# Optimization experiments

Measured on AMD Instinct MI355X. Metric: run time of the kernel, lower is better.

Reference implementation:

```python
import jax, jax.numpy as jnp
import numpy as np

B, S, H, E = 4, 2048, 1024, 8

def setup_inputs() -> dict:
    key = jax.random.key(0)
    k1, k2, k3 = jax.random.split(key, 3)
    scale_g = 1.0 / np.sqrt(H)
    scale_e = 1.0 / np.sqrt(H)
    return {
        "x": jax.random.normal(k1, (B, S, H), dtype=jnp.float32),
        "gate_w": jax.random.normal(k2, (H, E), dtype=jnp.float32) * scale_g,
        "gate_b": jnp.zeros((E,), dtype=jnp.float32),
        "expert_w": jax.random.normal(k3, (E, H, H), dtype=jnp.float32) * scale_e,
        "expert_b": jnp.zeros((E, H), dtype=jnp.float32),
    }

def reference(x, gate_w, gate_b, expert_w, expert_b):
    b, s, h = x.shape
    tok = x.reshape(-1, h)                                  # [T, H]
    # gate: softmax over experts per token
    w = jax.nn.softmax(tok @ gate_w + gate_b, axis=-1)      # [T, E]
    # all experts applied to all tokens (dense MoE)
    eo = jnp.einsum("th,ehd->ted", tok, expert_w) + expert_b[None]  # [T, E, H]
    out = jnp.einsum("te,ted->td", w, eo)                   # [T, H]
    return out.reshape(b, s, h)
```

## Files before the change

kernel.cpp:

```cpp
#include <hip/hip_runtime.h>
#include <stdint.h>

typedef unsigned short u16;
typedef short bf8 __attribute__((ext_vector_type(8)));
typedef float f4 __attribute__((ext_vector_type(4)));
typedef _Float16 h2 __attribute__((ext_vector_type(2)));

#define TTOK 8192
#define HD   1024
#define NE   8
#define HH   (HD * HD)

static __device__ __forceinline__ u16 f2bf(float f) {
  union { float f; uint32_t u; } v; v.f = f;
  return (u16)((v.u + 0x7fffu + ((v.u >> 16) & 1u)) >> 16);
}

__global__ __launch_bounds__(256) void gate_conv_kernel(
    const float* __restrict__ x, const float* __restrict__ gw,
    const float* __restrict__ gb, float* __restrict__ wout,
    u16* __restrict__ abf)
{
  const int t    = blockIdx.x * 4 + (threadIdx.x >> 6);
  const int lane = threadIdx.x & 63;
  const float* xr = x + (size_t)t * HD;
  float p[NE];
#pragma unroll
  for (int e = 0; e < NE; ++e) p[e] = 0.f;
#pragma unroll 4
  for (int h = lane; h < HD; h += 64) {
    const float xv = xr[h];
    abf[(size_t)t * HD + h] = f2bf(xv);
    const float* g = gw + (size_t)h * NE;
#pragma unroll
    for (int e = 0; e < NE; ++e) p[e] += xv * g[e];
  }
#pragma unroll
  for (int e = 0; e < NE; ++e) {
#pragma unroll
    for (int off = 32; off > 0; off >>= 1)
      p[e] += __shfl_xor(p[e], off, 64);
    p[e] += gb[e];
  }
  float m = p[0];
#pragma unroll
  for (int e = 1; e < NE; ++e) m = fmaxf(m, p[e]);
  float s = 0.f;
#pragma unroll
  for (int e = 0; e < NE; ++e) { p[e] = expf(p[e] - m); s += p[e]; }
  const float inv = 1.f / s;
  if (lane == 0) {
#pragma unroll
    for (int e = 0; e < NE; ++e) wout[t * NE + e] = p[e] * inv;
  }
}

__global__ __launch_bounds__(256) void wconv_kernel(
    const float* __restrict__ ew, u16* __restrict__ wt)
{
  __shared__ u16 tile[64][66];
  const int e  = blockIdx.z;
  const int h0 = blockIdx.y * 64;
  const int d0 = blockIdx.x * 64;
  const int c  = threadIdx.x & 63;
  const int r0 = threadIdx.x >> 6;
  const float* src = ew + (size_t)e * HH;
  u16* dst = wt + (size_t)e * HH;
#pragma unroll
  for (int i = 0; i < 16; ++i) {
    const int r = i * 4 + r0;
    tile[r][c] = f2bf(src[(size_t)(h0 + r) * HD + d0 + c]);
  }
  __syncthreads();
#pragma unroll
  for (int i = 0; i < 16; ++i) {
    const int r = i * 4 + r0;
    dst[(size_t)(d0 + r) * HD + h0 + c] = tile[c][r];
  }
}

#define BM 256
#define BN 128
#define BK 64
#define SLOT 65536

#define MM(a_, b_, c_) __builtin_amdgcn_mfma_f32_16x16x32_bf16((a_), (b_), (c_), 0, 0, 0)

#define GL(srcp_, dstp_) __builtin_amdgcn_global_load_lds( \
    (const __attribute__((address_space(1))) void*)(srcp_), \
    (__attribute__((address_space(3))) void*)(dstp_), 16, 0, 0)

#define STAGE_A(sq_)                                                \
  {                                                                 \
    const int sk_ = ((sq_) & 15) << 6;                              \
    const u16* as_ = aSrc0 + sk_;                                   \
    char* ad_ = smem + stS + tid * 16;                              \
    GL(as_,          ad_);                                          \
    GL(as_ +  65536, ad_ +  8192);                                  \
    GL(as_ + 131072, ad_ + 16384);                                  \
    GL(as_ + 196608, ad_ + 24576);                                  \
  }
#define STAGE_B(sq_)                                                \
  {                                                                 \
    const int pn_ = (sq_) >> 4;                                     \
    const int sk_ = ((sq_) & 15) << 6;                              \
    const u16* b0_ = bSrc0 + (size_t)(2 * pn_) * HH + sk_;          \
    char* bd_ = smem + stS + 32768 + tid * 16;                      \
    GL(b0_,          bd_);                                          \
    GL(b0_ +  65536, bd_ +  8192);                                  \
    GL(b0_ + HH,          bd_ + 16384);                             \
    GL(b0_ + HH + 65536,  bd_ + 24576);                             \
  }

#define READS(aP_, bP_)                                   \
    bf8 a0  = *(const bf8*)(aP_);                         \
    bf8 a1  = *(const bf8*)((aP_) + 2048);                \
    bf8 a2  = *(const bf8*)((aP_) + 4096);                \
    bf8 a3  = *(const bf8*)((aP_) + 6144);                \
    bf8 b00 = *(const bf8*)(bP_);                         \
    bf8 b01 = *(const bf8*)((bP_) + 2048);                \
    bf8 b02 = *(const bf8*)((bP_) + 4096);                \
    bf8 b03 = *(const bf8*)((bP_) + 6144);                \
    bf8 b10 = *(const bf8*)((bP_) + 16384);               \
    bf8 b11 = *(const bf8*)((bP_) + 18432);               \
    bf8 b12 = *(const bf8*)((bP_) + 20480);               \
    bf8 b13 = *(const bf8*)((bP_) + 22528);

#define MFMA32                                            \
    acc0[0][0] = MM(a0, b00, acc0[0][0]);                 \
    acc0[1][0] = MM(a1, b00, acc0[1][0]);                 \
    acc0[2][0] = MM(a2, b00, acc0[2][0]);                 \
    acc0[3][0] = MM(a3, b00, acc0[3][0]);                 \
    acc0[0][1] = MM(a0, b01, acc0[0][1]);                 \
    acc0[1][1] = MM(a1, b01, acc0[1][1]);                 \
    acc0[2][1] = MM(a2, b01, acc0[2][1]);                 \
    acc0[3][1] = MM(a3, b01, acc0[3][1]);                 \
    acc0[0][2] = MM(a0, b02, acc0[0][2]);                 \
    acc0[1][2] = MM(a1, b02, acc0[1][2]);                 \
    acc0[2][2] = MM(a2, b02, acc0[2][2]);                 \
    acc0[3][2] = MM(a3, b02, acc0[3][2]);                 \
    acc0[0][3] = MM(a0, b03, acc0[0][3]);                 \
    acc0[1][3] = MM(a1, b03, acc0[1][3]);                 \
    acc0[2][3] = MM(a2, b03, acc0[2][3]);                 \
    acc0[3][3] = MM(a3, b03, acc0[3][3]);                 \
    acc1[0][0] = MM(a0, b10, acc1[0][0]);                 \
    acc1[1][0] = MM(a1, b10, acc1[1][0]);                 \
    acc1[2][0] = MM(a2, b10, acc1[2][0]);                 \
    acc1[3][0] = MM(a3, b10, acc1[3][0]);                 \
    acc1[0][1] = MM(a0, b11, acc1[0][1]);                 \
    acc1[1][1] = MM(a1, b11, acc1[1][1]);                 \
    acc1[2][1] = MM(a2, b11, acc1[2][1]);                 \
    acc1[3][1] = MM(a3, b11, acc1[3][1]);                 \
    acc1[0][2] = MM(a0, b12, acc1[0][2]);                 \
    acc1[1][2] = MM(a1, b12, acc1[1][2]);                 \
    acc1[2][2] = MM(a2, b12, acc1[2][2]);                 \
    acc1[3][2] = MM(a3, b12, acc1[3][2]);                 \
    acc1[0][3] = MM(a0, b13, acc1[0][3]);                 \
    acc1[1][3] = MM(a1, b13, acc1[1][3]);                 \
    acc1[2][3] = MM(a2, b13, acc1[2][3]);                 \
    acc1[3][3] = MM(a3, b13, acc1[3][3]);

#define FOLD(e0_, e1_)                                                  \
  {                                                                     \
    _Pragma("unroll")                                                   \
    for (int mi = 0; mi < 4; ++mi) {                                    \
      const int r_ = wrb + mi * 16 + lhi * 4;                           \
      float wa[4], wb[4];                                               \
      _Pragma("unroll")                                                 \
      for (int j = 0; j < 4; ++j) {                                     \
        wa[j] = wgs[(r_ + j) * 9 + (e0_)];                              \
        wb[j] = wgs[(r_ + j) * 9 + (e1_)];                              \
      }                                                                 \
      _Pragma("unroll")                                                 \
      for (int ni = 0; ni < 4; ++ni) {                                  \
        const float f0 = wa[0] * acc0[mi][ni][0] + wb[0] * acc1[mi][ni][0]; \
        const float f1 = wa[1] * acc0[mi][ni][1] + wb[1] * acc1[mi][ni][1]; \
        const float f2 = wa[2] * acc0[mi][ni][2] + wb[2] * acc1[mi][ni][2]; \
        const float f3 = wa[3] * acc0[mi][ni][3] + wb[3] * acc1[mi][ni][3]; \
        h2 t0; t0[0] = (_Float16)f0; t0[1] = (_Float16)f1;              \
        h2 t1; t1[0] = (_Float16)f2; t1[1] = (_Float16)f3;              \
        accP0[mi][ni] += t0;                                            \
        accP1[mi][ni] += t1;                                            \
        acc0[mi][ni] = fz; acc1[mi][ni] = fz;                           \
      }                                                                 \
    }                                                                   \
  }

#define BAR       __builtin_amdgcn_s_barrier();
#define LGKM0     asm volatile("s_waitcnt lgkmcnt(0)" ::: "memory");
#define VM0       asm volatile("s_waitcnt vmcnt(0)" ::: "memory");
#define PRIO1     __builtin_amdgcn_s_setprio(1);
#define PRIO0     __builtin_amdgcn_s_setprio(0);

__global__ __launch_bounds__(512, 2) void moe_gemm_kernel(
    const u16* __restrict__ A,
    const u16* __restrict__ Wt,
    const float* __restrict__ wg,
    const float* __restrict__ eb,
    float* __restrict__ out)
{
  __shared__ __attribute__((aligned(16))) char smem[2 * SLOT + 9216];
  float* wgs = (float*)(smem + 2 * SLOT);

  const int bid   = blockIdx.x;
  const int xcd   = bid & 7;
  const int local = bid >> 3;
  const int bm    = xcd * 4 + (local & 3);
  const int bn    = local >> 2;
  const int row0  = bm * BM;
  const int col0  = bn * BN;

  const int tid  = threadIdx.x;
  const int lane = tid & 63;
  const int wid  = tid >> 6;
  const int wr   = wid >> 1;
  const int wc   = wid & 1;
  const int l15  = lane & 15;
  const int lhi  = lane >> 4;
  const int wrb  = wr * 64;
  const int wcb  = wc * 64;

  const int gsl   = (lhi ^ (l15 & 7)) << 4;
  const int thrA0 = wrb * 128 + l15 * 128 + gsl;
  const int thrA1 = thrA0 ^ 64;
  const int thrB0 = 32768 + wcb * 128 + l15 * 128 + gsl;
  const int thrB1 = thrB0 ^ 64;

  const int row_in = tid >> 3;
  const int gsw    = (tid & 7) ^ (row_in & 7);
  const u16* aSrc0 = A  + (size_t)(row0 + row_in) * HD + gsw * 8;
  const u16* bSrc0 = Wt + (size_t)(col0 + row_in) * HD + gsw * 8;

  {
    const f4 v = *(const f4*)(wg + (size_t)row0 * NE + tid * 4);
    const int i0 = tid * 4;
#pragma unroll
    for (int k = 0; k < 4; ++k) {
      const int idx = i0 + k;
      wgs[(idx >> 3) * 9 + (idx & 7)] = v[k];
    }
  }
  LGKM0

  const f4 fz = {0.f, 0.f, 0.f, 0.f};
  const h2 hz = {(_Float16)0.f, (_Float16)0.f};
  f4 acc0[4][4], acc1[4][4];
  h2 accP0[4][4], accP1[4][4];
#pragma unroll
  for (int i = 0; i < 4; ++i)
#pragma unroll
    for (int j = 0; j < 4; ++j) {
      acc0[i][j] = fz; acc1[i][j] = fz;
      accP0[i][j] = hz; accP1[i][j] = hz;
    }

  int curS = 0, stS = SLOT;

  { const int sv = stS; stS = 0; STAGE_A(0) STAGE_B(0) stS = sv; }

  for (int q = 0; q < 63; ++q) {
    VM0
    BAR
    const char* aP0 = smem + curS + thrA0;
    const char* aP1 = smem + curS + thrA1;
    const char* bP0 = smem + curS + thrB0;
    const char* bP1 = smem + curS + thrB1;
    {
      READS(aP0, bP0)
      STAGE_A(q + 1)
      BAR LGKM0 PRIO1
      MFMA32
      PRIO0 BAR
    }
    {
      READS(aP1, bP1)
      STAGE_B(q + 1)
      BAR LGKM0 PRIO1
      MFMA32
      PRIO0
    }
    { const int t_ = curS; curS = stS; stS = t_; }
    if ((q & 15) == 15) { const int p_ = q >> 4; FOLD(2 * p_, 2 * p_ + 1) }
  }
  VM0
  BAR
  {
    const char* aP0 = smem + curS + thrA0;
    const char* aP1 = smem + curS + thrA1;
    const char* bP0 = smem + curS + thrB0;
    const char* bP1 = smem + curS + thrB1;
    { READS(aP0, bP0) BAR LGKM0 PRIO1 MFMA32 PRIO0 BAR }
    { READS(aP1, bP1) BAR LGKM0 PRIO1 MFMA32 PRIO0 }
  }
  FOLD(6, 7)

  float ebv[4][8];
#pragma unroll
  for (int ni = 0; ni < 4; ++ni) {
    const int d = col0 + wcb + ni * 16 + l15;
#pragma unroll
    for (int e2 = 0; e2 < NE; ++e2) ebv[ni][e2] = eb[(size_t)e2 * HD + d];
  }
#pragma unroll
  for (int mi = 0; mi < 4; ++mi) {
    const int r_ = wrb + mi * 16 + lhi * 4;
#pragma unroll
    for (int j = 0; j < 4; ++j) {
      const int t = row0 + r_ + j;
      const float* wrow = &wgs[(r_ + j) * 9];
#pragma unroll
      for (int ni = 0; ni < 4; ++ni) {
        const float bias =
            wrow[0] * ebv[ni][0] + wrow[1] * ebv[ni][1] +
            wrow[2] * ebv[ni][2] + wrow[3] * ebv[ni][3] +
            wrow[4] * ebv[ni][4] + wrow[5] * ebv[ni][5] +
            wrow[6] * ebv[ni][6] + wrow[7] * ebv[ni][7];
        const float v = (j < 2) ? (float)accP0[mi][ni][j & 1]
                                : (float)accP1[mi][ni][j & 1];
        const int d = col0 + wcb + ni * 16 + l15;
        out[(size_t)t * HD + d] = v + bias;
      }
    }
  }
}

extern "C" void kernel_launch(void* const* d_in, const int* in_sizes, int n_in,
                              void* d_out, int out_size, void* d_ws, size_t ws_size,
                              hipStream_t stream) {
  const float* x  = (const float*)d_in[0];
  const float* gw = (const float*)d_in[1];
  const float* gb = (const float*)d_in[2];
  const float* ew = (const float*)d_in[3];
  const float* eb = (const float*)d_in[4];
  float* out = (float*)d_out;

  char* ws = (char*)d_ws;
  u16*   abf   = (u16*)ws;
  u16*   wt    = (u16*)(ws + (size_t)16 * 1024 * 1024);
  float* wgate = (float*)(ws + (size_t)32 * 1024 * 1024);

  gate_conv_kernel<<<dim3(TTOK / 4), dim3(256), 0, stream>>>(x, gw, gb, wgate, abf);
  wconv_kernel<<<dim3(16, 16, 8), dim3(256), 0, stream>>>(ew, wt);
  moe_gemm_kernel<<<dim3((TTOK / BM) * (HD / BN)), dim3(512), 0, stream>>>(abf, wt, wgate, eb, out);
}
```

Baseline: 140.2 us.

## Interleave LDS fragment reads with MFMA groups and drop intra-tile barriers

Replaces the per-half-tile pattern of reading all fragments, issuing a barrier, waiting for all LDS reads and then doing 32 MFMAs. Each tile now runs as four 16-MFMA groups, each gated by a partial lgkmcnt wait, so the next fragments load from LDS while the current MFMAs run. The two barriers inside each tile are removed, relying on double buffering plus the loop-top barrier for safety. Sched barriers pin the instruction order. The risks are higher register pressure from holding more fragments live and fragile hand-tuned wait counts.

```diff
diff --git a/kernel.cpp b/kernel.cpp
--- a/kernel.cpp
+++ b/kernel.cpp
@@ -112,53 +112,42 @@
     GL(b0_ + HH + 65536,  bd_ + 24576);                             \
   }
 
-#define READS(aP_, bP_)                                   \
-    bf8 a0  = *(const bf8*)(aP_);                         \
-    bf8 a1  = *(const bf8*)((aP_) + 2048);                \
-    bf8 a2  = *(const bf8*)((aP_) + 4096);                \
-    bf8 a3  = *(const bf8*)((aP_) + 6144);                \
-    bf8 b00 = *(const bf8*)(bP_);                         \
-    bf8 b01 = *(const bf8*)((bP_) + 2048);                \
-    bf8 b02 = *(const bf8*)((bP_) + 4096);                \
-    bf8 b03 = *(const bf8*)((bP_) + 6144);                \
-    bf8 b10 = *(const bf8*)((bP_) + 16384);               \
-    bf8 b11 = *(const bf8*)((bP_) + 18432);               \
-    bf8 b12 = *(const bf8*)((bP_) + 20480);               \
-    bf8 b13 = *(const bf8*)((bP_) + 22528);
-
-#define MFMA32                                            \
-    acc0[0][0] = MM(a0, b00, acc0[0][0]);                 \
-    acc0[1][0] = MM(a1, b00, acc0[1][0]);                 \
-    acc0[2][0] = MM(a2, b00, acc0[2][0]);                 \
-    acc0[3][0] = MM(a3, b00, acc0[3][0]);                 \
-    acc0[0][1] = MM(a0, b01, acc0[0][1]);                 \
-    acc0[1][1] = MM(a1, b01, acc0[1][1]);                 \
-    acc0[2][1] = MM(a2, b01, acc0[2][1]);                 \
-    acc0[3][1] = MM(a3, b01, acc0[3][1]);                 \
-    acc0[0][2] = MM(a0, b02, acc0[0][2]);                 \
-    acc0[1][2] = MM(a1, b02, acc0[1][2]);                 \
-    acc0[2][2] = MM(a2, b02, acc0[2][2]);                 \
-    acc0[3][2] = MM(a3, b02, acc0[3][2]);                 \
-    acc0[0][3] = MM(a0, b03, acc0[0][3]);                 \
-    acc0[1][3] = MM(a1, b03, acc0[1][3]);                 \
-    acc0[2][3] = MM(a2, b03, acc0[2][3]);                 \
-    acc0[3][3] = MM(a3, b03, acc0[3][3]);                 \
-    acc1[0][0] = MM(a0, b10, acc1[0][0]);                 \
-    acc1[1][0] = MM(a1, b10, acc1[1][0]);                 \
-    acc1[2][0] = MM(a2, b10, acc1[2][0]);                 \
-    acc1[3][0] = MM(a3, b10, acc1[3][0]);                 \
-    acc1[0][1] = MM(a0, b11, acc1[0][1]);                 \
-    acc1[1][1] = MM(a1, b11, acc1[1][1]);                 \
-    acc1[2][1] = MM(a2, b11, acc1[2][1]);                 \
-    acc1[3][1] = MM(a3, b11, acc1[3][1]);                 \
-    acc1[0][2] = MM(a0, b12, acc1[0][2]);                 \
-    acc1[1][2] = MM(a1, b12, acc1[1][2]);                 \
-    acc1[2][2] = MM(a2, b12, acc1[2][2]);                 \
-    acc1[3][2] = MM(a3, b12, acc1[3][2]);                 \
-    acc1[0][3] = MM(a0, b13, acc1[0][3]);                 \
-    acc1[1][3] = MM(a1, b13, acc1[1][3]);                 \
-    acc1[2][3] = MM(a2, b13, acc1[2][3]);                 \
-    acc1[3][3] = MM(a3, b13, acc1[3][3]);
+#define MFMA16E(ACC_, A0_, A1_, A2_, A3_, B0_, B1_, B2_, B3_)  \
+    ACC_[0][0] = MM(A0_, B0_, ACC_[0][0]);                     \
+    ACC_[1][0] = MM(A1_, B0_, ACC_[1][0]);                     \
+    ACC_[2][0] = MM(A2_, B0_, ACC_[2][0]);                     \
+    ACC_[3][0] = MM(A3_, B0_, ACC_[3][0]);                     \
+    ACC_[0][1] = MM(A0_, B1_, ACC_[0][1]);                     \
+    ACC_[1][1] = MM(A1_, B1_, ACC_[1][1]);                     \
+    ACC_[2][1] = MM(A2_, B1_, ACC_[2][1]);                     \
+    ACC_[3][1] = MM(A3_, B1_, ACC_[3][1]);                     \
+    ACC_[0][2] = MM(A0_, B2_, ACC_[0][2]);                     \
+    ACC_[1][2] = MM(A1_, B2_, ACC_[1][2]);                     \
+    ACC_[2][2] = MM(A2_, B2_, ACC_[2][2]);                     \
+    ACC_[3][2] = MM(A3_, B2_, ACC_[3][2]);                     \
+    ACC_[0][3] = MM(A0_, B3_, ACC_[0][3]);                     \
+    ACC_[1][3] = MM(A1_, B3_, ACC_[1][3]);                     \
+    ACC_[2][3] = MM(A3 == A3 ? A3_ : A3_, B3_, ACC_[2][3]);    \
+    ACC_[3][3] = MM(A3_, B3_, ACC_[3][3]);
+
+#undef MFMA16E
+#define MFMA16E(ACC_, A0_, A1_, A2_, A3_, B0_, B1_, B2_, B3_)  \
+    ACC_[0][0] = MM(A0_, B0_, ACC_[0][0]);                     \
+    ACC_[1][0] = MM(A1_, B0_, ACC_[1][0]);                     \
+    ACC_[2][0] = MM(A2_, B0_, ACC_[2][0]);                     \
+    ACC_[3][0] = MM(A3_, B0_, ACC_[3][0]);                     \
+    ACC_[0][1] = MM(A0_, B1_, ACC_[0][1]);                     \
+    ACC_[1][1] = MM(A1_, B1_, ACC_[1][1]);                     \
+    ACC_[2][1] = MM(A2_, B1_, ACC_[2][1]);                     \
+    ACC_[3][1] = MM(A3_, B1_, ACC_[3][1]);                     \
+    ACC_[0][2] = MM(A0_, B2_, ACC_[0][2]);                     \
+    ACC_[1][2] = MM(A1_, B2_, ACC_[1][2]);                     \
+    ACC_[2][2] = MM(A2_, B2_, ACC_[2][2]);                     \
+    ACC_[3][2] = MM(A3_, B2_, ACC_[3][2]);                     \
+    ACC_[0][3] = MM(A0_, B3_, ACC_[0][3]);                     \
+    ACC_[1][3] = MM(A1_, B3_, ACC_[1][3]);                     \
+    ACC_[2][3] = MM(A2_, B3_, ACC_[2][3]);                     \
+    ACC_[3][3] = MM(A3_, B3_, ACC_[3][3]);
 
 #define FOLD(e0_, e1_)                                                  \
   {                                                                     \
@@ -187,10 +176,61 @@
   }
 
 #define BAR       __builtin_amdgcn_s_barrier();
-#define LGKM0     asm volatile("s_waitcnt lgkmcnt(0)" ::: "memory");
 #define VM0       asm volatile("s_waitcnt vmcnt(0)" ::: "memory");
+#define LGKM(n_)  asm volatile("s_waitcnt lgkmcnt(" #n_ ")" ::: "memory");
+#define SCHED0    __builtin_amdgcn_sched_barrier(0);
 #define PRIO1     __builtin_amdgcn_s_setprio(1);
 #define PRIO0     __builtin_amdgcn_s_setprio(0);
+
+#define TILE_BODY(DO_STAGE_, sq_)                                        \
+  {                                                                      \
+    const char* aP0 = smem + curS + thrA0;                               \
+    const char* aP1 = smem + curS + thrA1;                               \
+    const char* bP0 = smem + curS + thrB0;                               \
+    const char* bP1 = smem + curS + thrB1;                               \
+                                       \
+    bf8 a00 = *(const bf8*)(aP0);                                        \
+    bf8 a01 = *(const bf8*)(aP0 + 2048);                                 \
+    bf8 a02 = *(const bf8*)(aP0 + 4096);                                 \
+    bf8 a03 = *(const bf8*)(aP0 + 6144);                                 \
+    bf8 b000 = *(const bf8*)(bP0);                                       \
+    bf8 b001 = *(const bf8*)(bP0 + 2048);                                \
+    bf8 b002 = *(const bf8*)(bP0 + 4096);                                \
+    bf8 b003 = *(const bf8*)(bP0 + 6144);                                \
+                          \
+    bf8 b100 = *(const bf8*)(bP0 + 16384);                               \
+    bf8 b101 = *(const bf8*)(bP0 + 18432);                               \
+    bf8 b102 = *(const bf8*)(bP0 + 20480);                               \
+    bf8 b103 = *(const bf8*)(bP0 + 22528);                               \
+    if (DO_STAGE_) STAGE_A(sq_)                                          \
+    LGKM(4) SCHED0                                                       \
+    PRIO1 MFMA16E(acc0, a00, a01, a02, a03, b000, b001, b002, b003)      \
+    PRIO0 SCHED0                                                         \
+              \
+    bf8 a10 = *(const bf8*)(aP1);                                        \
+    bf8 a11 = *(const bf8*)(aP1 + 2048);                                 \
+    bf8 a12 = *(const bf8*)(aP1 + 4096);                                 \
+    bf8 a13 = *(const bf8*)(aP1 + 6144);                                 \
+    bf8 b010 = *(const bf8*)(bP1);                                       \
+    bf8 b011 = *(const bf8*)(bP1 + 2048);                                \
+    bf8 b012 = *(const bf8*)(bP1 + 4096);                                \
+    bf8 b013 = *(const bf8*)(bP1 + 6144);                                \
+    LGKM(8) SCHED0                                                       \
+    PRIO1 MFMA16E(acc1, a00, a01, a02, a03, b100, b101, b102, b103)      \
+    PRIO0 SCHED0                                                         \
+    if (DO_STAGE_) STAGE_B(sq_)                                          \
+                          \
+    bf8 b110 = *(const bf8*)(bP1 + 16384);                               \
+    bf8 b111 = *(const bf8*)(bP1 + 18432);                               \
+    bf8 b112 = *(const bf8*)(bP1 + 20480);                               \
+    bf8 b113 = *(const bf8*)(bP1 + 22528);                               \
+    LGKM(4) SCHED0                                                       \
+    PRIO1 MFMA16E(acc0, a10, a11, a12, a13, b010, b011, b012, b013)      \
+    PRIO0 SCHED0                                                         \
+    LGKM(0) SCHED0                                                       \
+    PRIO1 MFMA16E(acc1, a10, a11, a12, a13, b110, b111, b112, b113)      \
+    PRIO0 SCHED0                                                         \
+  }
 
 __global__ __launch_bounds__(512, 2) void moe_gemm_kernel(
     const u16* __restrict__ A,
@@ -240,7 +280,7 @@
       wgs[(idx >> 3) * 9 + (idx & 7)] = v[k];
     }
   }
-  LGKM0
+  LGKM(0)
 
   const f4 fz = {0.f, 0.f, 0.f, 0.f};
   const h2 hz = {(_Float16)0.f, (_Float16)0.f};
@@ -261,37 +301,13 @@
   for (int q = 0; q < 63; ++q) {
     VM0
     BAR
-    const char* aP0 = smem + curS + thrA0;
-    const char* aP1 = smem + curS + thrA1;
-    const char* bP0 = smem + curS + thrB0;
-    const char* bP1 = smem + curS + thrB1;
-    {
-      READS(aP0, bP0)
-      STAGE_A(q + 1)
-      BAR LGKM0 PRIO1
-      MFMA32
-      PRIO0 BAR
-    }
-    {
-      READS(aP1, bP1)
-      STAGE_B(q + 1)
-      BAR LGKM0 PRIO1
-      MFMA32
-      PRIO0
-    }
+    TILE_BODY(1, q + 1)
     { const int t_ = curS; curS = stS; stS = t_; }
     if ((q & 15) == 15) { const int p_ = q >> 4; FOLD(2 * p_, 2 * p_ + 1) }
   }
   VM0
   BAR
-  {
-    const char* aP0 = smem + curS + thrA0;
-    const char* aP1 = smem + curS + thrA1;
-    const char* bP0 = smem + curS + thrB0;
-    const char* bP1 = smem + curS + thrB1;
-    { READS(aP0, bP0) BAR LGKM0 PRIO1 MFMA32 PRIO0 BAR }
-    { READS(aP1, bP1) BAR LGKM0 PRIO1 MFMA32 PRIO0 }
-  }
+  TILE_BODY(0, 0)
   FOLD(6, 7)
 
   float ebv[4][8];
```

Result: faster. 135.4 us (-3.5%).
